# Kernel optimization log

Measured on AMD Instinct MI355X. Metric: run time of the kernel, lower is better.

The kernel has to match this reference:

```python
import jax, jax.numpy as jnp
import numpy as np

K = 512      # model dim (= per-head dim in this module)
HEADS = 8
EPS = 1e-5


def layer_norm_2d(x, scale, offset):
    # haiku LayerNorm(axis=[-2,-1]): normalize over last two axes, per-feature params
    mean = jnp.mean(x, axis=(-2, -1), keepdims=True)
    var = jnp.var(x, axis=(-2, -1), keepdims=True)
    return scale * (x - mean) * jax.lax.rsqrt(var + EPS) + offset


def setup_inputs() -> dict:
    key = jax.random.key(0)
    ks = jax.random.split(key, 10)
    B, T, k, h = 4, 2048, K, HEADS
    s = lambda fan_in: 1.0 / np.sqrt(fan_in)
    return {
        "x": jax.random.normal(ks[0], (B, T, k), dtype=jnp.float32),
        "Wq": jax.random.normal(ks[1], (k, k * h), dtype=jnp.float32) * s(k),
        "Wk": jax.random.normal(ks[2], (k, k * h), dtype=jnp.float32) * s(k),
        "Wv": jax.random.normal(ks[3], (k, k * h), dtype=jnp.float32) * s(k),
        "Wu": jax.random.normal(ks[4], (k * h, k), dtype=jnp.float32) * s(k * h),
        "bu": jnp.zeros((k,), dtype=jnp.float32),
        "ln1_scale": jnp.ones((k,), dtype=jnp.float32),
        "ln1_offset": jnp.zeros((k,), dtype=jnp.float32),
        "W1": jax.random.normal(ks[5], (k, 4 * k), dtype=jnp.float32) * s(k),
        "b1": jnp.zeros((4 * k,), dtype=jnp.float32),
        "W2": jax.random.normal(ks[6], (4 * k, k), dtype=jnp.float32) * s(4 * k),
        "b2": jnp.zeros((k,), dtype=jnp.float32),
        "ln2_scale": jnp.ones((k,), dtype=jnp.float32),
        "ln2_offset": jnp.zeros((k,), dtype=jnp.float32),
    }


def reference(x, Wq, Wk, Wv, Wu, bu, ln1_scale, ln1_offset,
              W1, b1, W2, b2, ln2_scale, ln2_offset):
    B, T, k = x.shape
    h = HEADS
    # projections; '(k h)' split: head index is the FAST axis -> reshape (.., k, h)
    q = (x @ Wq).reshape(B, T, k, h)
    kk = (x @ Wk).reshape(B, T, k, h)
    v = (x @ Wv).reshape(B, T, k, h)
    scale = k ** (-0.25)
    q = q * scale
    kk = kk * scale
    # scores [B, h, T, T]
    dot = jnp.einsum('btkh,bskh->bhts', q, kk)
    dot = jax.nn.softmax(dot, axis=-1)
    # out '(b h) t k -> b t (h k)'
    out = jnp.einsum('bhts,bskh->bthk', dot, v).reshape(B, T, h * k)
    attn = out @ Wu + bu
    x = layer_norm_2d(attn, ln1_scale, ln1_offset) + x
    fwd = jax.nn.gelu(x @ W1 + b1)   # inference mode: dropout = 0
    fwd = fwd @ W2 + b2
    return layer_norm_2d(fwd + x, ln2_scale, ln2_offset)
```

## Files before the change

kernel.cpp:

```cpp
#include <hip/hip_runtime.h>
#include <cstdint>
#include <cstddef>

typedef uint16_t u16;
typedef uint32_t u32;
typedef __bf16 bf16x8 __attribute__((ext_vector_type(8)));
typedef float f32x4 __attribute__((ext_vector_type(4)));

#define TBLK 2048
#define KD 512
#define NH 8
#define MROWS 8192

__device__ __forceinline__ u16 f2b(float f){
  u32 u = __builtin_bit_cast(u32, f);
  u = (u + 0x7fffu + ((u >> 16) & 1u)) >> 16;
  return (u16)u;
}

__device__ __forceinline__ float gelu_tanh(float x){
  float x3 = x*x*x;
  float t = tanhf(0.7978845608028654f*(x + 0.044715f*x3));
  return 0.5f*x*(1.0f + t);
}

__device__ __forceinline__ void glds16(const u16* g, u16* l){
  __builtin_amdgcn_global_load_lds((const __attribute__((address_space(1))) void*)g,
                                   (__attribute__((address_space(3))) void*)l,
                                   16, 0, 0);
}

__global__ void to_bf16_kernel(const float* __restrict__ in, u16* __restrict__ out, int n4){
  int i = blockIdx.x*256 + threadIdx.x;
  if (i >= n4) return;
  size_t base = (size_t)i*4;
  float4 v = *(const float4*)(in + base);
  uint2 pk;
  pk.x = (u32)f2b(v.x) | ((u32)f2b(v.y) << 16);
  pk.y = (u32)f2b(v.z) | ((u32)f2b(v.w) << 16);
  *(uint2*)(out + base) = pk;
}

template<bool PERM>
__global__ void transpose_to_bf16(const float* __restrict__ in, u16* __restrict__ out, int R, int C){
  __shared__ float tile[64][65];
  int bc = blockIdx.x*64, br = blockIdx.y*64;
  int tx = threadIdx.x & 63, ty = threadIdx.x >> 6;
  #pragma unroll
  for (int i = 0; i < 64; i += 4)
    tile[ty+i][tx] = in[(size_t)(br+ty+i)*C + bc + tx];
  __syncthreads();
  #pragma unroll
  for (int i = 0; i < 64; i += 4){
    int n = bc + ty + i;
    int np = PERM ? ((n & 7)*512 + (n >> 3)) : n;
    out[(size_t)np*R + br + tx] = f2b(tile[tx][ty+i]);
  }
}

__global__ void transpose_qkv3(const float* __restrict__ wq, const float* __restrict__ wk,
                               const float* __restrict__ wv, u16* __restrict__ oq,
                               u16* __restrict__ ok, u16* __restrict__ ov){
  __shared__ float tile[64][65];
  const float* in = (blockIdx.z == 0) ? wq : (blockIdx.z == 1 ? wk : wv);
  u16* out = (blockIdx.z == 0) ? oq : (blockIdx.z == 1 ? ok : ov);
  int bc = blockIdx.x*64, br = blockIdx.y*64;
  int tx = threadIdx.x & 63, ty = threadIdx.x >> 6;
  #pragma unroll
  for (int i = 0; i < 64; i += 4)
    tile[ty+i][tx] = in[(size_t)(br+ty+i)*4096 + bc + tx];
  __syncthreads();
  #pragma unroll
  for (int i = 0; i < 64; i += 4){
    int n = bc + ty + i;
    int np = (n & 7)*512 + (n >> 3);
    out[(size_t)np*512 + br + tx] = f2b(tile[tx][ty+i]);
  }
}

template<int MODE, int BN>
__launch_bounds__(256, 2)
__global__ void gemm_bf16(const u16* __restrict__ A, int lda,
                          const u16* __restrict__ Bt, int M, int N, int K,
                          const float* __restrict__ bias, const float* __restrict__ resid,
                          float scale, u16* __restrict__ out16, float* __restrict__ out32,
                          u16* __restrict__ o2_16 = nullptr, u16* __restrict__ o3_16 = nullptr)
{
  __shared__ alignas(16) u16 At[2][128*32];
  __shared__ alignas(16) u16 Bs[2][BN*32];
  constexpr int MT = (BN == 128) ? 4 : 2;
  constexpr int BU = (BN == 128) ? 2 : 1;
  int ntn = N / BN;
  int tm = blockIdx.x / ntn;
  int tn = blockIdx.x - tm*ntn;
  int m0 = tm << 7, n0 = tn*BN;
  int tid = threadIdx.x;
  int lane = tid & 63;
  int w = tid >> 6;
  int wr = (BN == 128) ? (w >> 1) : w;
  int wc = (BN == 128) ? (w & 1) : 0;
  int rl = lane & 15, gr = lane >> 4;
  int srow = lane >> 2;
  int scol = (lane & 3) ^ ((lane >> 3) & 3);

  f32x4 acc[MT][4];
  #pragma unroll
  for (int m = 0; m < MT; ++m)
    #pragma unroll
    for (int n = 0; n < 4; ++n)
      #pragma unroll
      for (int r = 0; r < 4; ++r) acc[m][n][r] = 0.f;

  auto stage = [&](int buf, int k0){
    #pragma unroll
    for (int i = 0; i < 2; ++i){
      int u = w*2 + i;
      glds16(A + (size_t)(m0 + u*16 + srow)*lda + k0 + scol*8, &At[buf][u*512]);
    }
    #pragma unroll
    for (int i = 0; i < BU; ++i){
      int u = w*BU + i;
      glds16(Bt + (size_t)(n0 + u*16 + srow)*K + k0 + scol*8, &Bs[buf][u*512]);
    }
  };

  stage(0, 0);
  int nsteps = K >> 5;
  for (int s = 0; s < nsteps; ++s){
    int cur = s & 1;
    __syncthreads();
    if (s + 1 < nsteps) stage(cur ^ 1, (s + 1)*32);
    bf16x8 af[MT], bfv[4];
    #pragma unroll
    for (int m = 0; m < MT; ++m){
      int row = wr*MT*16 + m*16 + rl;
      af[m] = *(const bf16x8*)(&At[cur][row*32 + ((gr ^ ((row >> 1) & 3))*8)]);
    }
    #pragma unroll
    for (int n = 0; n < 4; ++n){
      int row = wc*64 + n*16 + rl;
      bfv[n] = *(const bf16x8*)(&Bs[cur][row*32 + ((gr ^ ((row >> 1) & 3))*8)]);
    }
    __builtin_amdgcn_s_setprio(1);
    #pragma unroll
    for (int m = 0; m < MT; ++m)
      #pragma unroll
      for (int n = 0; n < 4; ++n)
        acc[m][n] = __builtin_amdgcn_mfma_f32_16x16x32_bf16(af[m], bfv[n], acc[m][n], 0, 0, 0);
    __builtin_amdgcn_s_setprio(0);
  }

  #pragma unroll
  for (int m = 0; m < MT; ++m){
    #pragma unroll
    for (int n = 0; n < 4; ++n){
      int col = n0 + wc*64 + n*16 + rl;
      #pragma unroll
      for (int r = 0; r < 4; ++r){
        int row = m0 + wr*MT*16 + m*16 + gr*4 + r;
        float v = acc[m][n][r];
        if (MODE == 0){
          out16[(size_t)row*N + col] = f2b(v*scale);
        } else if (MODE == 2){
          out32[(size_t)row*512 + col] = v + bias[col];
        } else if (MODE == 3){
          out16[(size_t)row*2048 + col] = f2b(gelu_tanh(v + bias[col]));
        } else if (MODE == 4){
          out32[(size_t)row*512 + col] = v + bias[col] + resid[(size_t)row*512 + col];
        } else {
          u16* dst = (col < 4096) ? out16 : (col < 8192 ? o2_16 : o3_16);
          float sc = (col < 8192) ? scale : 1.0f;
          dst[(size_t)row*4096 + (col & 4095)] = f2b(v*sc);
        }
      }
    }
  }
}

__global__ void vtrans_kernel(const u16* __restrict__ vg, u16* __restrict__ vtb){
  __shared__ alignas(16) u16 tile[64][72];
  int t0 = blockIdx.x*64;
  int d0 = blockIdx.y*64;
  int bh = blockIdx.z;
  int bl = bh >> 3, h = bh & 7;
  int tid = threadIdx.x;
  #pragma unroll
  for (int it = 0; it < 4; ++it){
    int id = it*256 + tid;
    int r = id >> 4, cq = id & 15;
    *(uint2*)(&tile[r][cq*4]) =
        *(const uint2*)(vg + (size_t)(bl*TBLK + t0 + r)*4096 + h*512 + d0 + cq*4);
  }
  __syncthreads();
  #pragma unroll
  for (int it = 0; it < 2; ++it){
    int id = it*256 + tid;
    int dr = id >> 3, tg = id & 7;
    alignas(16) u16 tmp[8];
    #pragma unroll
    for (int j = 0; j < 8; ++j) tmp[j] = tile[tg*8 + j][dr];
    *(uint4*)(vtb + ((size_t)bh*512 + d0 + dr)*TBLK + t0 + tg*8) = *(const uint4*)tmp;
  }
}

__launch_bounds__(512, 2)
__global__ void flash_attn(const u16* __restrict__ qg, const u16* __restrict__ kg,
                           const u16* __restrict__ vtb, u16* __restrict__ ctx)
{
  int bh = blockIdx.x;
  int qt = blockIdx.y;
  int bl = bh >> 3, h = bh & 7;
  int tid = threadIdx.x;
  int lane = tid & 63, w = tid >> 6;
  int rl = lane & 15, gr = lane >> 4;
  const u16* Qb = qg + (size_t)bl*TBLK*4096 + h*512;
  const u16* Kb = kg + (size_t)bl*TBLK*4096 + h*512;
  const u16* Vb = vtb + (size_t)bh*512*TBLK;

  __shared__ alignas(16) u16 Ka[2][32*512];
  __shared__ alignas(16) u16 Va[2][512*32];
  __shared__ alignas(16) u16 Pl[8][512];

  int q0 = qt*128 + w*16;
  bf16x8 qf[16];
  #pragma unroll
  for (int kc = 0; kc < 16; ++kc)
    qf[kc] = *(const bf16x8*)(Qb + (size_t)(q0 + rl)*4096 + kc*32 + gr*8);

  f32x4 o[32];
  #pragma unroll
  for (int n = 0; n < 32; ++n)
    #pragma unroll
    for (int r = 0; r < 4; ++r) o[n][r] = 0.f;
  float mrow[4] = {-1e30f, -1e30f, -1e30f, -1e30f};
  float lsum[4] = {0.f, 0.f, 0.f, 0.f};

  auto stage = [&](int buf, int s0){
    #pragma unroll
    for (int i = 0; i < 4; ++i){
      int wl = w*4 + i;
      glds16(Kb + (size_t)(s0 + wl)*4096 + (size_t)((lane ^ (wl & 7))*8),
             &Ka[buf][wl*512]);
      int d = wl*16 + (lane >> 2);
      int oj = (lane & 3) ^ ((d >> 1) & 3);
      glds16(Vb + (size_t)d*TBLK + s0 + oj*8,
             &Va[buf][wl*512]);
    }
  };

  stage(0, 0);

  for (int t = 0; t < 64; ++t){
    int cur = t & 1;
    __syncthreads();

    f32x4 sA[2];
    #pragma unroll
    for (int n = 0; n < 2; ++n)
      #pragma unroll
      for (int r = 0; r < 4; ++r) sA[n][r] = 0.f;
    __builtin_amdgcn_s_setprio(1);
    #pragma unroll
    for (int kc = 0; kc < 16; ++kc){
      #pragma unroll
      for (int n = 0; n < 2; ++n){
        int rowS = n*16 + rl;
        bf16x8 kf = *(const bf16x8*)(&Ka[cur][rowS*512 + (((kc*4 + gr) ^ (rowS & 7))*8)]);
        sA[n] = __builtin_amdgcn_mfma_f32_16x16x32_bf16(qf[kc], kf, sA[n], 0, 0, 0);
      }
    }
    __builtin_amdgcn_s_setprio(0);

    if (t < 63) stage(cur ^ 1, (t + 1)*32);

    bool updl = false;
    #pragma unroll
    for (int n = 0; n < 2; ++n)
      #pragma unroll
      for (int r = 0; r < 4; ++r) updl |= (sA[n][r] > mrow[r] + 8.0f);
    if (__any(updl)){
      float pm[4], fr[4];
      #pragma unroll
      for (int r = 0; r < 4; ++r) pm[r] = fmaxf(sA[0][r], sA[1][r]);
      #pragma unroll
      for (int m = 1; m < 16; m <<= 1)
        #pragma unroll
        for (int r = 0; r < 4; ++r) pm[r] = fmaxf(pm[r], __shfl_xor(pm[r], m));
      #pragma unroll
      for (int r = 0; r < 4; ++r){
        float mn = fmaxf(mrow[r], pm[r]);
        fr[r] = __expf(mrow[r] - mn);
        mrow[r] = mn;
        lsum[r] *= fr[r];
      }
      #pragma unroll
      for (int n = 0; n < 32; ++n)
        #pragma unroll
        for (int r = 0; r < 4; ++r) o[n][r] *= fr[r];
    }

    float p0[4], p1[4];
    #pragma unroll
    for (int r = 0; r < 4; ++r){
      p0[r] = __expf(sA[0][r] - mrow[r]);
      p1[r] = __expf(sA[1][r] - mrow[r]);
      lsum[r] += p0[r] + p1[r];
    }

    u16* pw = &Pl[w][0];
    #pragma unroll
    for (int r = 0; r < 4; ++r){
      int tq = gr*4 + r;
      pw[tq*32 + rl]      = f2b(p0[r]);
      pw[tq*32 + 16 + rl] = f2b(p1[r]);
    }
    asm volatile("s_waitcnt lgkmcnt(0)" ::: "memory");
    bf16x8 pa = *(const bf16x8*)(pw + rl*32 + gr*8);

    __builtin_amdgcn_s_setprio(1);
    #pragma unroll
    for (int n = 0; n < 32; ++n){
      int rowV = n*16 + rl;
      bf16x8 vf = *(const bf16x8*)(&Va[cur][rowV*32 + ((gr ^ ((rowV >> 1) & 3))*8)]);
      o[n] = __builtin_amdgcn_mfma_f32_16x16x32_bf16(pa, vf, o[n], 0, 0, 0);
    }
    __builtin_amdgcn_s_setprio(0);
  }

  #pragma unroll
  for (int m = 1; m < 16; m <<= 1)
    #pragma unroll
    for (int r = 0; r < 4; ++r) lsum[r] += __shfl_xor(lsum[r], m);

  #pragma unroll
  for (int n = 0; n < 32; ++n){
    int d = n*16 + rl;
    #pragma unroll
    for (int r = 0; r < 4; ++r){
      int tq = q0 + gr*4 + r;
      float v = o[n][r] / lsum[r];
      ctx[((size_t)(bl*TBLK + tq))*4096 + h*512 + d] = f2b(v);
    }
  }
}

__global__ void reduce_ms(const float* __restrict__ in, float* __restrict__ part, int nblk){
  int b = blockIdx.y;
  const float4* p = (const float4*)(in + (size_t)b*TBLK*KD);
  int n4 = TBLK*KD/4;
  float s = 0.f, s2 = 0.f;
  for (int i = blockIdx.x*blockDim.x + threadIdx.x; i < n4; i += nblk*blockDim.x){
    float4 v = p[i];
    s  += v.x + v.y + v.z + v.w;
    s2 += v.x*v.x + v.y*v.y + v.z*v.z + v.w*v.w;
  }
  #pragma unroll
  for (int m = 1; m < 64; m <<= 1){ s += __shfl_xor(s, m); s2 += __shfl_xor(s2, m); }
  __shared__ float sh[8];
  int w = threadIdx.x >> 6;
  if ((threadIdx.x & 63) == 0){ sh[w] = s; sh[4 + w] = s2; }
  __syncthreads();
  if (threadIdx.x == 0){
    float a = 0.f, a2 = 0.f;
    for (int i = 0; i < 4; ++i){ a += sh[i]; a2 += sh[4 + i]; }
    part[((size_t)b*nblk + blockIdx.x)*2]     = a;
    part[((size_t)b*nblk + blockIdx.x)*2 + 1] = a2;
  }
}

__global__ void finalize_ms(const float* __restrict__ part, float* __restrict__ stats, int nblk){
  int b = blockIdx.x;
  float s = 0.f, s2 = 0.f;
  for (int i = threadIdx.x; i < nblk; i += 64){
    s  += part[((size_t)b*nblk + i)*2];
    s2 += part[((size_t)b*nblk + i)*2 + 1];
  }
  #pragma unroll
  for (int m = 1; m < 64; m <<= 1){ s += __shfl_xor(s, m); s2 += __shfl_xor(s2, m); }
  if (threadIdx.x == 0){
    float inv_n = 1.0f/((float)TBLK*KD);
    float mean = s*inv_n;
    float var = s2*inv_n - mean*mean;
    stats[b*2] = mean;
    stats[b*2 + 1] = 1.0f/sqrtf(var + 1e-5f);
  }
}

__global__ void ln1_apply(const float* __restrict__ attn, const float* __restrict__ x,
                          const float* __restrict__ stats, const float* __restrict__ gs,
                          const float* __restrict__ go, float* __restrict__ x1f,
                          u16* __restrict__ x1b){
  int g = blockIdx.x*256 + threadIdx.x;
  size_t base = (size_t)g*4;
  int b = (int)(base >> 20);
  int col = (int)(base & (KD - 1));
  float mean = stats[b*2], inv = stats[b*2 + 1];
  float4 a  = *(const float4*)(attn + base);
  float4 xr = *(const float4*)(x + base);
  float4 sc = *(const float4*)(gs + col);
  float4 of = *(const float4*)(go + col);
  float4 r;
  r.x = sc.x*(a.x - mean)*inv + of.x + xr.x;
  r.y = sc.y*(a.y - mean)*inv + of.y + xr.y;
  r.z = sc.z*(a.z - mean)*inv + of.z + xr.z;
  r.w = sc.w*(a.w - mean)*inv + of.w + xr.w;
  *(float4*)(x1f + base) = r;
  uint2 pk;
  pk.x = (u32)f2b(r.x) | ((u32)f2b(r.y) << 16);
  pk.y = (u32)f2b(r.z) | ((u32)f2b(r.w) << 16);
  *(uint2*)(x1b + base) = pk;
}

__global__ void ln2_apply(const float* __restrict__ y, const float* __restrict__ stats,
                          const float* __restrict__ gs, const float* __restrict__ go,
                          float* __restrict__ outp){
  int g = blockIdx.x*256 + threadIdx.x;
  size_t base = (size_t)g*4;
  int b = (int)(base >> 20);
  int col = (int)(base & (KD - 1));
  float mean = stats[b*2], inv = stats[b*2 + 1];
  float4 v  = *(const float4*)(y + base);
  float4 sc = *(const float4*)(gs + col);
  float4 of = *(const float4*)(go + col);
  float4 r;
  r.x = sc.x*(v.x - mean)*inv + of.x;
  r.y = sc.y*(v.y - mean)*inv + of.y;
  r.z = sc.z*(v.z - mean)*inv + of.z;
  r.w = sc.w*(v.w - mean)*inv + of.w;
  *(float4*)(outp + base) = r;
}

extern "C" void kernel_launch(void* const* d_in, const int* in_sizes, int n_in,
                              void* d_out, int out_size, void* d_ws, size_t ws_size,
                              hipStream_t stream)
{
  const float* x  = (const float*)d_in[0];
  const float* Wq = (const float*)d_in[1];
  const float* Wk = (const float*)d_in[2];
  const float* Wv = (const float*)d_in[3];
  const float* Wu = (const float*)d_in[4];
  const float* bu = (const float*)d_in[5];
  const float* g1 = (const float*)d_in[6];
  const float* o1 = (const float*)d_in[7];
  const float* W1 = (const float*)d_in[8];
  const float* b1 = (const float*)d_in[9];
  const float* W2 = (const float*)d_in[10];
  const float* b2 = (const float*)d_in[11];
  const float* g2 = (const float*)d_in[12];
  const float* o2 = (const float*)d_in[13];
  float* outp = (float*)d_out;
  (void)in_sizes; (void)n_in; (void)out_size;

  char* ws = (char*)d_ws;
  size_t off = 0;
  auto take = [&](size_t bytes)->char*{
    char* p = ws + off; off += (bytes + 255) & ~(size_t)255; return p;
  };
  u16* x16 = (u16*)take((size_t)MROWS*KD*2);
  u16* wqt = (u16*)take((size_t)4096*512*2);
  u16* wkt = (u16*)take((size_t)4096*512*2);
  u16* wvt = (u16*)take((size_t)4096*512*2);
  u16* wut = (u16*)take((size_t)512*4096*2);
  u16* w1t = (u16*)take((size_t)2048*512*2);
  u16* w2t = (u16*)take((size_t)512*2048*2);
  float* red = (float*)take((size_t)(4*256*2 + 8)*4);
  float* stats = red + 4*256*2;
  size_t fixed_end = off;

  size_t need1 = fixed_end + 4*((size_t)8192*8192 + 256);
  int cm = (ws_size >= need1) ? 8192 : 4096;
  int nchunks = MROWS / cm;
  size_t big = (size_t)cm*8192;
  u16* qg  = (u16*)take(big);
  u16* kg  = (u16*)take(big);
  u16* vg  = (u16*)take(big);
  u16* vtb = (u16*)take(big);

  u16* ctx    = vg;
  char* qgc   = (char*)qg;
  float* attn = (float*)qgc;
  float* x1f  = (float*)(qgc + (size_t)cm*2048);
  u16*   x1b  = (u16*) (qgc + (size_t)cm*4096);
  float* yb   = (float*)(qgc + (size_t)cm*5120);
  u16*   fwd  = kg;

  const float qscale = 0.21022410381342865f;

  to_bf16_kernel<<<dim3(4096), dim3(256), 0, stream>>>(x, x16, MROWS*KD/4);
  transpose_qkv3<<<dim3(64, 8, 3), dim3(256), 0, stream>>>(Wq, Wk, Wv, wqt, wkt, wvt);
  transpose_to_bf16<false><<<dim3(8, 64), dim3(256), 0, stream>>>(Wu, wut, 4096, 512);
  transpose_to_bf16<false><<<dim3(32, 8), dim3(256), 0, stream>>>(W1, w1t, 512, 2048);
  transpose_to_bf16<false><<<dim3(8, 32), dim3(256), 0, stream>>>(W2, w2t, 2048, 512);

  int nb = cm / TBLK;
  int nbh = nb * NH;
  for (int chunk = 0; chunk < nchunks; ++chunk){
    const u16* xc  = x16 + (size_t)chunk*cm*KD;
    const float* xf = x  + (size_t)chunk*cm*KD;

    gemm_bf16<5,128><<<dim3((cm/128)*96), dim3(256), 0, stream>>>(xc, 512, wqt, cm, 12288, 512,
                                                        nullptr, nullptr, qscale, qg, nullptr,
                                                        kg, vg);
    vtrans_kernel<<<dim3(32, 8, nbh), dim3(256), 0, stream>>>(vg, vtb);
    flash_attn<<<dim3(nbh, 16), dim3(512), 0, stream>>>(qg, kg, vtb, ctx);

    gemm_bf16<2,64><<<dim3((cm/128)*8), dim3(256), 0, stream>>>(ctx, 4096, wut, cm, 512, 4096,
                                                       bu, nullptr, 1.0f, nullptr, attn);
    reduce_ms<<<dim3(256, nb), dim3(256), 0, stream>>>(attn, red, 256);
    finalize_ms<<<dim3(nb), dim3(64), 0, stream>>>(red, stats, 256);
    ln1_apply<<<dim3(cm/2), dim3(256), 0, stream>>>(attn, xf, stats, g1, o1, x1f, x1b);

    gemm_bf16<3,128><<<dim3((cm/128)*16), dim3(256), 0, stream>>>(x1b, 512, w1t, cm, 2048, 512,
                                                        b1, nullptr, 1.0f, fwd, nullptr);
    gemm_bf16<4,64><<<dim3((cm/128)*8), dim3(256), 0, stream>>>(fwd, 2048, w2t, cm, 512, 2048,
                                                       b2, x1f, 1.0f, nullptr, yb);
    reduce_ms<<<dim3(256, nb), dim3(256), 0, stream>>>(yb, red, 256);
    finalize_ms<<<dim3(nb), dim3(64), 0, stream>>>(red, stats, 256);
    ln2_apply<<<dim3(cm/2), dim3(256), 0, stream>>>(yb, stats, g2, o2, outp + (size_t)chunk*cm*KD);
  }
}
```

Baseline: 867.3 us.

## Store V and softmax probabilities in fp8 and use fp8 MFMA for PV

The QKV projection epilogue now writes V as fp8. The V transpose kernel produces an fp8 layout pre-tiled for MFMA fragment loads. Flash attention stages that layout and computes P·V with the fp8×fp8 16x16x32 MFMA, storing P in fp8 in LDS. This halves V memory and LDS traffic and uses the higher-rate fp8 matrix path, at the cost of reduced precision in the attention output; the lazy-rescale threshold is tightened to keep P within fp8 range.

Result: faster. 761.7 us, median of 2 (-12.2%).

```diff
diff --git a/kernel.cpp b/kernel.cpp
--- a/kernel.cpp
+++ b/kernel.cpp
@@ -4,6 +4,8 @@
 
 typedef uint16_t u16;
 typedef uint32_t u32;
+typedef unsigned char u8;
+typedef long long i64;
 typedef __bf16 bf16x8 __attribute__((ext_vector_type(8)));
 typedef float f32x4 __attribute__((ext_vector_type(4)));
 
@@ -18,13 +20,17 @@
   return (u16)u;
 }
 
+__device__ __forceinline__ u8 f2fp8(float f){
+  return (u8)(__builtin_amdgcn_cvt_pk_fp8_f32(f, f, 0, false) & 0xff);
+}
+
 __device__ __forceinline__ float gelu_tanh(float x){
   float x3 = x*x*x;
   float t = tanhf(0.7978845608028654f*(x + 0.044715f*x3));
   return 0.5f*x*(1.0f + t);
 }
 
-__device__ __forceinline__ void glds16(const u16* g, u16* l){
+__device__ __forceinline__ void glds16(const void* g, void* l){
   __builtin_amdgcn_global_load_lds((const __attribute__((address_space(1))) void*)g,
                                    (__attribute__((address_space(3))) void*)l,
                                    16, 0, 0);
@@ -84,7 +90,7 @@
                           const u16* __restrict__ Bt, int M, int N, int K,
                           const float* __restrict__ bias, const float* __restrict__ resid,
                           float scale, u16* __restrict__ out16, float* __restrict__ out32,
-                          u16* __restrict__ o2_16 = nullptr, u16* __restrict__ o3_16 = nullptr)
+                          u16* __restrict__ k16 = nullptr, u8* __restrict__ v8 = nullptr)
 {
   __shared__ alignas(16) u16 At[2][128*32];
   __shared__ alignas(16) u16 Bs[2][BN*32];
@@ -159,53 +165,53 @@
       for (int r = 0; r < 4; ++r){
         int row = m0 + wr*MT*16 + m*16 + gr*4 + r;
         float v = acc[m][n][r];
-        if (MODE == 0){
-          out16[(size_t)row*N + col] = f2b(v*scale);
-        } else if (MODE == 2){
+        if (MODE == 2){
           out32[(size_t)row*512 + col] = v + bias[col];
         } else if (MODE == 3){
           out16[(size_t)row*2048 + col] = f2b(gelu_tanh(v + bias[col]));
         } else if (MODE == 4){
           out32[(size_t)row*512 + col] = v + bias[col] + resid[(size_t)row*512 + col];
         } else {
-          u16* dst = (col < 4096) ? out16 : (col < 8192 ? o2_16 : o3_16);
-          float sc = (col < 8192) ? scale : 1.0f;
-          dst[(size_t)row*4096 + (col & 4095)] = f2b(v*sc);
+          if (col < 4096)       out16[(size_t)row*4096 + col]          = f2b(v*scale);
+          else if (col < 8192)  k16[(size_t)row*4096 + (col & 4095)]   = f2b(v*scale);
+          else                  v8[(size_t)row*4096 + (col & 4095)]    = f2fp8(v);
         }
       }
     }
   }
 }
 
-__global__ void vtrans_kernel(const u16* __restrict__ vg, u16* __restrict__ vtb){
-  __shared__ alignas(16) u16 tile[64][72];
+__global__ void vtrans_kernel(const u8* __restrict__ vg8, u8* __restrict__ vt8){
+  __shared__ alignas(16) u8 tile[64][80];
   int t0 = blockIdx.x*64;
   int d0 = blockIdx.y*64;
   int bh = blockIdx.z;
   int bl = bh >> 3, h = bh & 7;
   int tid = threadIdx.x;
-  #pragma unroll
-  for (int it = 0; it < 4; ++it){
-    int id = it*256 + tid;
-    int r = id >> 4, cq = id & 15;
-    *(uint2*)(&tile[r][cq*4]) =
-        *(const uint2*)(vg + (size_t)(bl*TBLK + t0 + r)*4096 + h*512 + d0 + cq*4);
+  {
+    int row = tid >> 2, cb = (tid & 3)*16;
+    *(uint4*)(&tile[row][cb]) =
+        *(const uint4*)(vg8 + (size_t)(bl*TBLK + t0 + row)*4096 + h*512 + d0 + cb);
   }
   __syncthreads();
   #pragma unroll
   for (int it = 0; it < 2; ++it){
-    int id = it*256 + tid;
-    int dr = id >> 3, tg = id & 7;
-    alignas(16) u16 tmp[8];
-    #pragma unroll
-    for (int j = 0; j < 8; ++j) tmp[j] = tile[tg*8 + j][dr];
-    *(uint4*)(vtb + ((size_t)bh*512 + d0 + dr)*TBLK + t0 + tg*8) = *(const uint4*)tmp;
+    int o = it*256 + tid;
+    int rl = o & 15, gr = (o >> 4) & 3, gl = (o >> 6) & 3, st2 = (o >> 8) & 1;
+    int d_local = gl*16 + rl;
+    int tb = st2*32 + gr*8;
+    alignas(8) u8 tmp[8];
+    #pragma unroll
+    for (int j = 0; j < 8; ++j) tmp[j] = tile[tb + j][d_local];
+    size_t region = ((size_t)bh*64 + (t0 >> 5) + st2)*16384;
+    int g = (d0 >> 4) + gl;
+    *(uint2*)(vt8 + region + g*512 + gr*128 + rl*8) = *(const uint2*)tmp;
   }
 }
 
 __launch_bounds__(512, 2)
 __global__ void flash_attn(const u16* __restrict__ qg, const u16* __restrict__ kg,
-                           const u16* __restrict__ vtb, u16* __restrict__ ctx)
+                           const u8* __restrict__ vt8, u16* __restrict__ ctx)
 {
   int bh = blockIdx.x;
   int qt = blockIdx.y;
@@ -215,11 +221,11 @@
   int rl = lane & 15, gr = lane >> 4;
   const u16* Qb = qg + (size_t)bl*TBLK*4096 + h*512;
   const u16* Kb = kg + (size_t)bl*TBLK*4096 + h*512;
-  const u16* Vb = vtb + (size_t)bh*512*TBLK;
+  const u8*  Vb = vt8 + (size_t)bh*64*16384;
 
   __shared__ alignas(16) u16 Ka[2][32*512];
-  __shared__ alignas(16) u16 Va[2][512*32];
-  __shared__ alignas(16) u16 Pl[8][512];
+  __shared__ alignas(16) u8  Va[2][16384];
+  __shared__ alignas(16) u8  Pl[8][640];
 
   int q0 = qt*128 + w*16;
   bf16x8 qf[16];
@@ -241,10 +247,11 @@
       int wl = w*4 + i;
       glds16(Kb + (size_t)(s0 + wl)*4096 + (size_t)((lane ^ (wl & 7))*8),
              &Ka[buf][wl*512]);
-      int d = wl*16 + (lane >> 2);
-      int oj = (lane & 3) ^ ((d >> 1) & 3);
-      glds16(Vb + (size_t)d*TBLK + s0 + oj*8,
-             &Va[buf][wl*512]);
+    }
+    #pragma unroll
+    for (int i = 0; i < 2; ++i){
+      int u = w*2 + i;
+      glds16(Vb + (size_t)(s0 >> 5)*16384 + u*1024 + lane*16, &Va[buf][u*1024]);
     }
   };
 
@@ -277,7 +284,7 @@
     #pragma unroll
     for (int n = 0; n < 2; ++n)
       #pragma unroll
-      for (int r = 0; r < 4; ++r) updl |= (sA[n][r] > mrow[r] + 8.0f);
+      for (int r = 0; r < 4; ++r) updl |= (sA[n][r] > mrow[r] + 5.0f);
     if (__any(updl)){
       float pm[4], fr[4];
       #pragma unroll
@@ -307,22 +314,21 @@
       lsum[r] += p0[r] + p1[r];
     }
 
-    u16* pw = &Pl[w][0];
+    u8* pw = &Pl[w][0];
     #pragma unroll
     for (int r = 0; r < 4; ++r){
       int tq = gr*4 + r;
-      pw[tq*32 + rl]      = f2b(p0[r]);
-      pw[tq*32 + 16 + rl] = f2b(p1[r]);
+      pw[tq*40 + rl]      = f2fp8(p0[r]);
+      pw[tq*40 + 16 + rl] = f2fp8(p1[r]);
     }
     asm volatile("s_waitcnt lgkmcnt(0)" ::: "memory");
-    bf16x8 pa = *(const bf16x8*)(pw + rl*32 + gr*8);
+    i64 pa = *(const i64*)(pw + rl*40 + gr*8);
 
     __builtin_amdgcn_s_setprio(1);
     #pragma unroll
     for (int n = 0; n < 32; ++n){
-      int rowV = n*16 + rl;
-      bf16x8 vf = *(const bf16x8*)(&Va[cur][rowV*32 + ((gr ^ ((rowV >> 1) & 3))*8)]);
-      o[n] = __builtin_amdgcn_mfma_f32_16x16x32_bf16(pa, vf, o[n], 0, 0, 0);
+      i64 vf = *(const i64*)(&Va[cur][n*512 + gr*128 + rl*8]);
+      o[n] = __builtin_amdgcn_mfma_f32_16x16x32_fp8_fp8(pa, vf, o[n], 0, 0, 0);
     }
     __builtin_amdgcn_s_setprio(0);
   }
@@ -467,21 +473,20 @@
   float* stats = red + 4*256*2;
   size_t fixed_end = off;
 
-  size_t need1 = fixed_end + 4*((size_t)8192*8192 + 256);
+  size_t need1 = fixed_end + (size_t)8192*32768 + 4096;
   int cm = (ws_size >= need1) ? 8192 : 4096;
   int nchunks = MROWS / cm;
-  size_t big = (size_t)cm*8192;
-  u16* qg  = (u16*)take(big);
-  u16* kg  = (u16*)take(big);
-  u16* vg  = (u16*)take(big);
-  u16* vtb = (u16*)take(big);
-
-  u16* ctx    = vg;
-  char* qgc   = (char*)qg;
-  float* attn = (float*)qgc;
-  float* x1f  = (float*)(qgc + (size_t)cm*2048);
-  u16*   x1b  = (u16*) (qgc + (size_t)cm*4096);
-  float* yb   = (float*)(qgc + (size_t)cm*5120);
+  u16* qg  = (u16*)take((size_t)cm*8192);
+  u16* kg  = (u16*)take((size_t)cm*8192);
+  u8*  vg8 = (u8*)take((size_t)cm*4096);
+  u8*  vt8 = (u8*)take((size_t)cm*4096);
+  u16* ctx = (u16*)take((size_t)cm*8192);
+
+  char* qc = (char*)qg;
+  float* attn = (float*)qc;
+  float* x1f  = (float*)(qc + (size_t)cm*2048);
+  u16*   x1b  = (u16*) (qc + (size_t)cm*4096);
+  float* yb   = (float*)(qc + (size_t)cm*5120);
   u16*   fwd  = kg;
 
   const float qscale = 0.21022410381342865f;
@@ -499,10 +504,10 @@
     const float* xf = x  + (size_t)chunk*cm*KD;
 
     gemm_bf16<5,128><<<dim3((cm/128)*96), dim3(256), 0, stream>>>(xc, 512, wqt, cm, 12288, 512,
-                                                        nullptr, nullptr, qscale, qg, nullptr,
-                                                        kg, vg);
-    vtrans_kernel<<<dim3(32, 8, nbh), dim3(256), 0, stream>>>(vg, vtb);
-    flash_attn<<<dim3(nbh, 16), dim3(512), 0, stream>>>(qg, kg, vtb, ctx);
+                                                        nullptr, nullptr, qscale,
+                                                        qg, nullptr, kg, vg8);
+    vtrans_kernel<<<dim3(32, 8, nbh), dim3(256), 0, stream>>>(vg8, vt8);
+    flash_attn<<<dim3(nbh, 16), dim3(512), 0, stream>>>(qg, kg, vt8, ctx);
 
     gemm_bf16<2,64><<<dim3((cm/128)*8), dim3(256), 0, stream>>>(ctx, 4096, wut, cm, 512, 4096,
                                                        bu, nullptr, 1.0f, nullptr, attn);
```
